# Optimization experiments

Measured on AMD Instinct MI355X. Metric: run time of the kernel, lower is better.

Reference implementation:

```python
import jax, jax.numpy as jnp
import numpy as np


def setup_inputs() -> dict:
    key = jax.random.key(0)
    k1, k2, k3 = jax.random.split(key, 3)
    B, V, J = 32, 100000, 52
    vertices = jax.random.normal(k1, (1, V, 3), dtype=jnp.float32)
    lbs_weights = jax.random.uniform(k2, (1, V, J), dtype=jnp.float32)
    skinning_transforms = jax.random.normal(k3, (B, J, 4, 4), dtype=jnp.float32)
    return {
        "vertices": vertices,
        "lbs_weights": lbs_weights,
        "skinning_transforms": skinning_transforms,
    }


def reference(vertices, lbs_weights, skinning_transforms):
    # 3D-vertices branch of Skinning.forward
    B = skinning_transforms.shape[0]
    J = skinning_transforms.shape[1]
    V = vertices.shape[1]
    # W: [B,V,J] (broadcast of [1,V,J]); T_flat: [B,V,16] -> T: [B,V,4,4]
    T = jnp.einsum(
        "bvj,bjx->bvx",
        jnp.broadcast_to(lbs_weights, (B, V, J)),
        skinning_transforms.reshape(B, J, 16),
    ).reshape(B, V, 4, 4)
    # homogeneous vertex coords [B,V,4]
    v_posed_homo = jnp.concatenate(
        [
            jnp.broadcast_to(vertices, (B, V, 3)),
            jnp.ones((B, V, 1), dtype=vertices.dtype),
        ],
        axis=2,
    )
    # per-vertex 4x4 @ 4 transform, keep xyz
    v_homo = jnp.einsum("bvij,bvj->bvi", T, v_posed_homo)
    return v_homo[:, :, :3]
```

## Files before the change

kernel.cpp:

```cpp
#include <hip/hip_runtime.h>
#include <hip/hip_bf16.h>


typedef __attribute__((ext_vector_type(8))) short bf16x8;
typedef __attribute__((ext_vector_type(4))) float f32x4;

constexpr int J      = 52;
constexpr int KSTEPS = 7;
constexpr int NT     = 6;
constexpr int WAVES  = 4;
constexpr int MT     = 2;
constexpr int VPW    = MT * 16;
constexpr int VPB    = WAVES * VPW;
constexpr int NSLOT  = KSTEPS * NT * 64;
constexpr int BP_B   = NSLOT * 16;
constexpr int OUT_B  = 16 * VPB * 3 * 4;

typedef const __attribute__((address_space(1))) char* gas1_t;
typedef __attribute__((address_space(3))) char* las3_t;

__device__ __forceinline__ unsigned pk2(float a, float b) {
    __hip_bfloat162 h = __float22bfloat162_rn(make_float2(a, b));
    return *reinterpret_cast<unsigned*>(&h);
}

__global__ __launch_bounds__(256) void pack_A(
    const float* __restrict__ xf,
    bf16x8* __restrict__ Bp)
{
    const int slot = blockIdx.x * 256 + threadIdx.x;
    if (slot >= NSLOT) return;
    const int s    = slot / (NT * 64);
    const int rem  = slot - s * (NT * 64);
    const int t    = rem >> 6;
    const int l    = rem & 63;
    const int lgrp = l >> 4;
    const int lrow = l & 15;
    const int n = t * 16 + lrow;
    const int b = n / 3;
    const int i = n - 3 * b;
    const int j0 = s * 8 + lgrp * 2;
    const float4* __restrict__ xf4 = reinterpret_cast<const float4*>(xf);
    float4 m0 = {0,0,0,0}, m1 = {0,0,0,0};
    if (j0 < J)     m0 = xf4[(b * J + j0) * 4 + i];
    if (j0 + 1 < J) m1 = xf4[(b * J + j0 + 1) * 4 + i];
    union { bf16x8 v; unsigned w[4]; } r;
    r.w[0] = pk2(m0.x, m0.y); r.w[1] = pk2(m0.z, m0.w);
    r.w[2] = pk2(m1.x, m1.y); r.w[3] = pk2(m1.z, m1.w);
    Bp[slot] = r.v;
}

__global__ __launch_bounds__(256, 2) void skin_mfma(
    const float* __restrict__ verts,
    const float* __restrict__ weights,
    const bf16x8* __restrict__ Bp,
    float* __restrict__ out,
    int V)
{
    __shared__ __align__(16) char sBp[BP_B];
    __shared__ __align__(16) char sOut[OUT_B];

    const int tid  = threadIdx.x;
    const int lane = tid & 63;
    const int wid  = tid >> 6;
    const int lgrp = lane >> 4;
    const int lrow = lane & 15;
    const int v0   = blockIdx.x * VPB;

    {
        const char* g = (const char*)Bp;
        for (int p = wid; p < BP_B / 1024; p += WAVES) {
            __builtin_amdgcn_global_load_lds(
                (gas1_t)(g + p * 1024 + lane * 16),
                (las3_t)(sBp + p * 1024), 16, 0, 0);
        }
    }

    float hx[MT], hy[MT], hz[MT];
    float2 wv[MT][KSTEPS];
#pragma unroll
    for (int mt = 0; mt < MT; ++mt) {
        const int v   = v0 + wid * VPW + mt * 16 + lrow;
        const int vcl = (v < V) ? v : (V - 1);
        hx[mt] = verts[3 * (size_t)vcl + 0];
        hy[mt] = verts[3 * (size_t)vcl + 1];
        hz[mt] = verts[3 * (size_t)vcl + 2];
        const float* wr = weights + (size_t)vcl * J;
#pragma unroll
        for (int s = 0; s < KSTEPS; ++s) {
            const int j0 = s * 8 + lgrp * 2;
            wv[mt][s] = (j0 < J) ? *(const float2*)(wr + j0) : float2{0.f, 0.f};
        }
    }

    __syncthreads();

    f32x4 acc[MT][NT];
#pragma unroll
    for (int mt = 0; mt < MT; ++mt)
#pragma unroll
        for (int t = 0; t < NT; ++t)
            acc[mt][t] = f32x4{0.f, 0.f, 0.f, 0.f};

#pragma unroll
    for (int s = 0; s < KSTEPS; ++s) {
        bf16x8 frag[NT];
#pragma unroll
        for (int t = 0; t < NT; ++t)
            frag[t] = *(const bf16x8*)(sBp + ((s * NT + t) * 64 + lane) * 16);
#pragma unroll
        for (int mt = 0; mt < MT; ++mt) {
            const float w0 = wv[mt][s].x, w1 = wv[mt][s].y;
            union { bf16x8 v; unsigned w[4]; } xf8;
            xf8.w[0] = pk2(w0 * hx[mt], w0 * hy[mt]);
            xf8.w[1] = pk2(w0 * hz[mt], w0);
            xf8.w[2] = pk2(w1 * hx[mt], w1 * hy[mt]);
            xf8.w[3] = pk2(w1 * hz[mt], w1);
#pragma unroll
            for (int t = 0; t < NT; ++t) {
                acc[mt][t] = __builtin_amdgcn_mfma_f32_16x16x32_bf16(
                    frag[t], xf8.v, acc[mt][t], 0, 0, 0);
            }
        }
    }

    const long long validf = ((long long)V - v0) * 3;
#pragma unroll
    for (int h = 0; h < 2; ++h) {
        __syncthreads();
#pragma unroll
        for (int mt = 0; mt < MT; ++mt) {
            const int vloc = wid * VPW + mt * 16 + lrow;
#pragma unroll
            for (int tt = 0; tt < 3; ++tt) {
                const int t = 3 * h + tt;
#pragma unroll
                for (int r = 0; r < 4; ++r) {
                    const int n  = 16 * t + lgrp * 4 + r;
                    const int b  = n / 3;
                    const int i  = n - 3 * b;
                    const int fl = ((b - 16 * h) * VPB + vloc) * 3 + i;
                    *(float*)(sOut + fl * 4) = acc[mt][t][r];
                }
            }
        }
        __syncthreads();
#pragma unroll
        for (int q = 0; q < 6; ++q) {
            const int idx = q * 256 + tid;
            const int bl  = idx / 96;
            const int rr  = idx - bl * 96;
            const f32x4 val = *(const f32x4*)(sOut + (bl * 96 + rr) * 16);
            if ((long long)rr * 4 + 4 <= validf) {
                const int b = 16 * h + bl;
                float4* dst = (float4*)(out + (size_t)b * (size_t)V * 3
                                            + (size_t)v0 * 3) + rr;
                *dst = *(const float4*)&val;
            }
        }
    }
}

extern "C" void kernel_launch(void* const* d_in, const int* in_sizes, int n_in,
                              void* d_out, int out_size, void* d_ws, size_t ws_size,
                              hipStream_t stream)
{
    const float* verts   = (const float*)d_in[0];
    const float* weights = (const float*)d_in[1];
    const float* xf      = (const float*)d_in[2];
    float* out = (float*)d_out;

    const int V = in_sizes[0] / 3;
    bf16x8* Bp = (bf16x8*)d_ws;

    pack_A<<<(NSLOT + 255) / 256, 256, 0, stream>>>(xf, Bp);
    const int nblocks = (V + VPB - 1) / VPB;
    skin_mfma<<<nblocks, 256, 0, stream>>>(verts, weights, Bp, out, V);
}
```

Baseline: 25.90 us.

## Fuse transform packing into skinning kernel and use per-wave output staging

Removes the separate pack_A launch: each block now reads the skinning transforms from global memory, converts them to bf16 and writes the MFMA fragment layout into LDS itself. The output epilogue switches from block-wide LDS staging with __syncthreads to per-wave staging slices synchronised with waitcnt, and adds a scalar tail path for partial float4s. This saves one kernel launch and the block barriers in the epilogue, but every block now repeats the transform load and bf16 conversion work.

```diff
diff --git a/kernel.cpp b/kernel.cpp
--- a/kernel.cpp
+++ b/kernel.cpp
@@ -14,51 +14,22 @@
 constexpr int VPB    = WAVES * VPW;
 constexpr int NSLOT  = KSTEPS * NT * 64;
 constexpr int BP_B   = NSLOT * 16;
-constexpr int OUT_B  = 16 * VPB * 3 * 4;
-
-typedef const __attribute__((address_space(1))) char* gas1_t;
-typedef __attribute__((address_space(3))) char* las3_t;
+constexpr int SL_B   = 16 * VPW * 3 * 4;
 
 __device__ __forceinline__ unsigned pk2(float a, float b) {
     __hip_bfloat162 h = __float22bfloat162_rn(make_float2(a, b));
     return *reinterpret_cast<unsigned*>(&h);
 }
 
-__global__ __launch_bounds__(256) void pack_A(
-    const float* __restrict__ xf,
-    bf16x8* __restrict__ Bp)
-{
-    const int slot = blockIdx.x * 256 + threadIdx.x;
-    if (slot >= NSLOT) return;
-    const int s    = slot / (NT * 64);
-    const int rem  = slot - s * (NT * 64);
-    const int t    = rem >> 6;
-    const int l    = rem & 63;
-    const int lgrp = l >> 4;
-    const int lrow = l & 15;
-    const int n = t * 16 + lrow;
-    const int b = n / 3;
-    const int i = n - 3 * b;
-    const int j0 = s * 8 + lgrp * 2;
-    const float4* __restrict__ xf4 = reinterpret_cast<const float4*>(xf);
-    float4 m0 = {0,0,0,0}, m1 = {0,0,0,0};
-    if (j0 < J)     m0 = xf4[(b * J + j0) * 4 + i];
-    if (j0 + 1 < J) m1 = xf4[(b * J + j0 + 1) * 4 + i];
-    union { bf16x8 v; unsigned w[4]; } r;
-    r.w[0] = pk2(m0.x, m0.y); r.w[1] = pk2(m0.z, m0.w);
-    r.w[2] = pk2(m1.x, m1.y); r.w[3] = pk2(m1.z, m1.w);
-    Bp[slot] = r.v;
-}
-
-__global__ __launch_bounds__(256, 2) void skin_mfma(
+__global__ __launch_bounds__(256, 2) void skin_fused(
     const float* __restrict__ verts,
     const float* __restrict__ weights,
-    const bf16x8* __restrict__ Bp,
+    const float* __restrict__ xf,
     float* __restrict__ out,
     int V)
 {
     __shared__ __align__(16) char sBp[BP_B];
-    __shared__ __align__(16) char sOut[OUT_B];
+    __shared__ __align__(16) char sSl[WAVES][SL_B];
 
     const int tid  = threadIdx.x;
     const int lane = tid & 63;
@@ -66,21 +37,13 @@
     const int lgrp = lane >> 4;
     const int lrow = lane & 15;
     const int v0   = blockIdx.x * VPB;
-
-    {
-        const char* g = (const char*)Bp;
-        for (int p = wid; p < BP_B / 1024; p += WAVES) {
-            __builtin_amdgcn_global_load_lds(
-                (gas1_t)(g + p * 1024 + lane * 16),
-                (las3_t)(sBp + p * 1024), 16, 0, 0);
-        }
-    }
+    const int v0w  = v0 + wid * VPW;
 
     float hx[MT], hy[MT], hz[MT];
     float2 wv[MT][KSTEPS];
 #pragma unroll
     for (int mt = 0; mt < MT; ++mt) {
-        const int v   = v0 + wid * VPW + mt * 16 + lrow;
+        const int v   = v0w + mt * 16 + lrow;
         const int vcl = (v < V) ? v : (V - 1);
         hx[mt] = verts[3 * (size_t)vcl + 0];
         hy[mt] = verts[3 * (size_t)vcl + 1];
@@ -93,6 +56,28 @@
         }
     }
 
+    {
+        const float4* __restrict__ xf4 = reinterpret_cast<const float4*>(xf);
+        for (int slot = tid; slot < NSLOT; slot += 256) {
+            const int s     = slot / (NT * 64);
+            const int rem   = slot - s * (NT * 64);
+            const int t     = rem >> 6;
+            const int l     = rem & 63;
+            const int plgrp = l >> 4;
+            const int plrow = l & 15;
+            const int n  = t * 16 + plrow;
+            const int b  = n / 3;
+            const int i  = n - 3 * b;
+            const int j0 = s * 8 + plgrp * 2;
+            float4 m0 = {0,0,0,0}, m1 = {0,0,0,0};
+            if (j0 < J)     m0 = xf4[(b * J + j0) * 4 + i];
+            if (j0 + 1 < J) m1 = xf4[(b * J + j0 + 1) * 4 + i];
+            union { bf16x8 v; unsigned w[4]; } r;
+            r.w[0] = pk2(m0.x, m0.y); r.w[1] = pk2(m0.z, m0.w);
+            r.w[2] = pk2(m1.x, m1.y); r.w[3] = pk2(m1.z, m1.w);
+            *(bf16x8*)(sBp + slot * 16) = r.v;
+        }
+    }
     __syncthreads();
 
     f32x4 acc[MT][NT];
@@ -124,13 +109,13 @@
         }
     }
 
-    const long long validf = ((long long)V - v0) * 3;
+    char* const sl = sSl[wid];
+    const long long validf = ((long long)V - v0w) * 3;
 #pragma unroll
     for (int h = 0; h < 2; ++h) {
-        __syncthreads();
 #pragma unroll
         for (int mt = 0; mt < MT; ++mt) {
-            const int vloc = wid * VPW + mt * 16 + lrow;
+            const int vloc = mt * 16 + lrow;
 #pragma unroll
             for (int tt = 0; tt < 3; ++tt) {
                 const int t = 3 * h + tt;
@@ -139,23 +124,36 @@
                     const int n  = 16 * t + lgrp * 4 + r;
                     const int b  = n / 3;
                     const int i  = n - 3 * b;
-                    const int fl = ((b - 16 * h) * VPB + vloc) * 3 + i;
-                    *(float*)(sOut + fl * 4) = acc[mt][t][r];
+                    const int fl = ((b - 16 * h) * VPW + vloc) * 3 + i;
+                    *(float*)(sl + fl * 4) = acc[mt][t][r];
                 }
             }
         }
-        __syncthreads();
+        asm volatile("s_waitcnt lgkmcnt(0)" ::: "memory");
+        __builtin_amdgcn_sched_barrier(0);
+
+        f32x4 vals[6];
 #pragma unroll
         for (int q = 0; q < 6; ++q) {
-            const int idx = q * 256 + tid;
-            const int bl  = idx / 96;
-            const int rr  = idx - bl * 96;
-            const f32x4 val = *(const f32x4*)(sOut + (bl * 96 + rr) * 16);
-            if ((long long)rr * 4 + 4 <= validf) {
-                const int b = 16 * h + bl;
-                float4* dst = (float4*)(out + (size_t)b * (size_t)V * 3
-                                            + (size_t)v0 * 3) + rr;
-                *dst = *(const float4*)&val;
+            const int f = q * 64 + lane;
+            vals[q] = *(const f32x4*)(sl + f * 16);
+        }
+        asm volatile("s_waitcnt lgkmcnt(0)" ::: "memory");
+        __builtin_amdgcn_sched_barrier(0);
+
+#pragma unroll
+        for (int q = 0; q < 6; ++q) {
+            const int f  = q * 64 + lane;
+            const int bl = f / 24;
+            const int rr = f - bl * 24;
+            float* dst = out + (size_t)(16 * h + bl) * (size_t)V * 3
+                             + (size_t)v0w * 3 + rr * 4;
+            if ((long long)(rr + 1) * 4 <= validf) {
+                *(float4*)dst = *(const float4*)&vals[q];
+            } else if ((long long)rr * 4 < validf) {
+#pragma unroll
+                for (int e = 0; e < 4; ++e)
+                    if ((long long)(rr * 4 + e) < validf) dst[e] = vals[q][e];
             }
         }
     }
@@ -171,9 +169,6 @@
     float* out = (float*)d_out;
 
     const int V = in_sizes[0] / 3;
-    bf16x8* Bp = (bf16x8*)d_ws;
-
-    pack_A<<<(NSLOT + 255) / 256, 256, 0, stream>>>(xf, Bp);
     const int nblocks = (V + VPB - 1) / VPB;
-    skin_mfma<<<nblocks, 256, 0, stream>>>(verts, weights, Bp, out, V);
+    skin_fused<<<nblocks, 256, 0, stream>>>(verts, weights, xf, out, V);
 }
```

Result: slower. 29.26 us (+13.0%).
